# Optimization experiments

Hardware: AMD Instinct MI355X
Metric: run time of the kernel (lower is better)

The kernel has to match this reference:

```python
import jax, jax.numpy as jnp
import numpy as np

NUM_HEADS = 16

def setup_inputs() -> dict:
    key = jax.random.key(0)
    k1, k2, k3 = jax.random.split(key, 3)
    B, N, C = 4, 4096, 1024
    x = jax.random.normal(k1, (B, N, C), dtype=jnp.float32)
    y = jax.random.normal(k2, (B, N, C), dtype=jnp.float32)
    # nn.Linear(embed_dim, embed_dim): weight [C, C], bias [C]
    W_proj = jax.random.normal(k3, (C, C), dtype=jnp.float32) * (1.0 / np.sqrt(C))
    b_proj = jnp.zeros((C,), dtype=jnp.float32)
    return {"x": x, "y": y, "W_proj": W_proj, "b_proj": b_proj}

def reference(x, y, W_proj, b_proj):
    B, N, C = x.shape
    H = NUM_HEADS
    d = C // H
    # NOTE: no head transpose in the original -> scores are over the HEAD axis.
    q = x.reshape(B, N, H, d)
    k = y.reshape(B, N, H, d)
    v = y.reshape(B, N, H, d)
    # attn: [B, N, H, H], per-token head-to-head scores
    attn = jnp.einsum('bnhd,bngd->bnhg', q, k) / jnp.sqrt(jnp.asarray(d, x.dtype))
    attn = jax.nn.softmax(attn, axis=-1)
    # dropout(p=0.1) is identity in eval mode
    o = jnp.einsum('bnhg,bngd->bnhd', attn, v)          # [B, N, H, d]
    # x.transpose(1, 2).reshape(B, N, C) in torch:
    o = jnp.transpose(o, (0, 2, 1, 3)).reshape(B, N, C)
    out = o @ W_proj.T + b_proj
    return out
```

## Files before the change

### kernel.cpp

```cpp
#include <hip/hip_runtime.h>
#include <hip/hip_bf16.h>
#include <stdint.h>

typedef __attribute__((ext_vector_type(8))) short bf16x8;
typedef __attribute__((ext_vector_type(4))) short bf16x4;
typedef __attribute__((ext_vector_type(4))) float f32x4;
typedef __attribute__((ext_vector_type(4))) int   i32x4;

static __device__ __forceinline__ short f2bs(float f) {
  __hip_bfloat16 h = __float2bfloat16(f);
  return __builtin_bit_cast(short, h);
}

__device__ __forceinline__ void gload_lds16(const void* g, void* l) {
  auto* gp = reinterpret_cast<__attribute__((address_space(1))) uint32_t*>((uintptr_t)g);
  auto* lp = reinterpret_cast<__attribute__((address_space(3))) uint32_t*>((uintptr_t)l);
  __builtin_amdgcn_global_load_lds(gp, lp, 16, 0, 0);
}

__global__ __launch_bounds__(256) void attn_kernel(
    const float* __restrict__ x, const float* __restrict__ y,
    __hip_bfloat16* __restrict__ A)
{
  const int wid  = threadIdx.x >> 6;
  const int lane = threadIdx.x & 63;
  const int tok  = blockIdx.x * 4 + wid;
  const int b    = tok >> 12;
  const int n    = tok & 4095;

  const float* xr = x + (size_t)tok * 1024;
  const float* yr = y + (size_t)tok * 1024;

  const int c  = lane & 15;
  const int qq = lane >> 4;

  const int fbase = c * 64 + qq * 8;
  bf16x8 yf[2], xf[2];
  #pragma unroll
  for (int kk = 0; kk < 2; ++kk) {
    const float4 a0 = *(const float4*)(yr + fbase + kk * 32);
    const float4 a1 = *(const float4*)(yr + fbase + kk * 32 + 4);
    const float4 b0 = *(const float4*)(xr + fbase + kk * 32);
    const float4 b1 = *(const float4*)(xr + fbase + kk * 32 + 4);
    yf[kk] = bf16x8{f2bs(a0.x), f2bs(a0.y), f2bs(a0.z), f2bs(a0.w),
                    f2bs(a1.x), f2bs(a1.y), f2bs(a1.z), f2bs(a1.w)};
    xf[kk] = bf16x8{f2bs(b0.x), f2bs(b0.y), f2bs(b0.z), f2bs(b0.w),
                    f2bs(b1.x), f2bs(b1.y), f2bs(b1.z), f2bs(b1.w)};
  }

  f32x4 acc = {0.f, 0.f, 0.f, 0.f};
  acc = __builtin_amdgcn_mfma_f32_16x16x32_bf16(yf[0], xf[0], acc, 0, 0, 0);
  acc = __builtin_amdgcn_mfma_f32_16x16x32_bf16(yf[1], xf[1], acc, 0, 0, 0);

  float sc[4];
  #pragma unroll
  for (int r = 0; r < 4; ++r) sc[r] = acc[r] * 0.125f;
  float mx = fmaxf(fmaxf(sc[0], sc[1]), fmaxf(sc[2], sc[3]));
  mx = fmaxf(mx, __shfl_xor(mx, 16));
  mx = fmaxf(mx, __shfl_xor(mx, 32));
  float e[4];
  #pragma unroll
  for (int r = 0; r < 4; ++r) e[r] = __expf(sc[r] - mx);
  float sm = (e[0] + e[1]) + (e[2] + e[3]);
  sm += __shfl_xor(sm, 16);
  sm += __shfl_xor(sm, 32);
  const float inv = 1.0f / sm;
  float p[4];
  #pragma unroll
  for (int r = 0; r < 4; ++r) p[r] = e[r] * inv;

  f32x4 o[4];
  #pragma unroll
  for (int q = 0; q < 4; ++q) o[q] = f32x4{0.f, 0.f, 0.f, 0.f};

#if __has_builtin(__builtin_amdgcn_mfma_f32_16x16x16bf16_1k)
  const bf16x4 pa = {f2bs(p[0]), f2bs(p[1]), f2bs(p[2]), f2bs(p[3])};
  #pragma unroll
  for (int q = 0; q < 4; ++q) {
    bf16x4 bq;
    #pragma unroll
    for (int j = 0; j < 4; ++j)
      bq[j] = f2bs(yr[(qq * 4 + j) * 64 + q * 16 + c]);
    o[q] = __builtin_amdgcn_mfma_f32_16x16x16bf16_1k(pa, bq, o[q], 0, 0, 0);
  }
#else
  const int u0 = ((int)(unsigned short)f2bs(p[1]) << 16) | (unsigned short)f2bs(p[0]);
  const int u1 = ((int)(unsigned short)f2bs(p[3]) << 16) | (unsigned short)f2bs(p[2]);
  const int s0 = c + 32 * qq;
  int a0 = __shfl(u0, s0), a1 = __shfl(u1, s0);
  int a2 = __shfl(u0, s0 + 16), a3 = __shfl(u1, s0 + 16);
  const bool valid = (qq < 2);
  if (!valid) { a0 = 0; a1 = 0; a2 = 0; a3 = 0; }
  const bf16x8 a8 = __builtin_bit_cast(bf16x8, i32x4{a0, a1, a2, a3});
  #pragma unroll
  for (int q = 0; q < 4; ++q) {
    bf16x8 b8;
    #pragma unroll
    for (int j = 0; j < 8; ++j) {
      const int g = (qq * 8 + j) & 15;
      const float v = yr[g * 64 + q * 16 + c];
      b8[j] = valid ? f2bs(v) : (short)0;
    }
    o[q] = __builtin_amdgcn_mfma_f32_16x16x32_bf16(a8, b8, o[q], 0, 0, 0);
  }
#endif

  const size_t base = ((size_t)b * 4096 + (n >> 4)) * 1024 + ((n & 15) << 6) + c;
  #pragma unroll
  for (int q = 0; q < 4; ++q)
    #pragma unroll
    for (int r = 0; r < 4; ++r) {
      const int h = qq * 4 + r;
      A[base + (size_t)h * 262144 + q * 16] = __float2bfloat16(o[q][r]);
    }
}

__global__ __launch_bounds__(256) void wcvt_kernel(const float* __restrict__ w,
                                                   __hip_bfloat16* __restrict__ wb)
{
  const int i = (blockIdx.x * 256 + threadIdx.x) * 4;
  const float4 v = *(const float4*)(w + i);
  wb[i + 0] = __float2bfloat16(v.x);
  wb[i + 1] = __float2bfloat16(v.y);
  wb[i + 2] = __float2bfloat16(v.z);
  wb[i + 3] = __float2bfloat16(v.w);
}

#define NT 32

#define FENCE asm volatile("" ::: "memory")
#define BAR   __builtin_amdgcn_s_barrier()
#define LGKM0 asm volatile("s_waitcnt lgkmcnt(0)" ::: "memory")
#define VM4   asm volatile("s_waitcnt vmcnt(4)" ::: "memory")
#define VM0   asm volatile("s_waitcnt vmcnt(0)" ::: "memory")
#define SB0   __builtin_amdgcn_sched_barrier(0)
#define SP1   __builtin_amdgcn_s_setprio(1)
#define SP0   __builtin_amdgcn_s_setprio(0)

#define STAGE(toff, bo) do {                                        \
    gload_lds16(aSrc + (toff),          aDst + (bo));               \
    gload_lds16(aSrc + (toff) + 131072, aDst + (bo) + 4096);        \
    gload_lds16(bSrc + (toff),          bDst + (bo));               \
    gload_lds16(bSrc + (toff) + 131072, bDst + (bo) + 4096);        \
  } while (0)

__global__ __launch_bounds__(256, 3) void gemm128(
    const __hip_bfloat16* __restrict__ A,
    const __hip_bfloat16* __restrict__ Bw,
    const float* __restrict__ bias,
    float* __restrict__ C)
{
  constexpr int K = 1024, Nn = 1024;
  __shared__ char ldsA[3 * 8192];
  __shared__ char ldsB[3 * 8192];

  const int tid  = threadIdx.x;
  const int lane = tid & 63;
  const int wid  = tid >> 6;
  const int wr   = wid >> 1;
  const int wcN  = wid & 1;

  const int bid = blockIdx.x;
  const int nb  = (bid & 7) * 128 + (bid >> 3);
  const int mBase = (nb >> 3) * 128;
  const int nBase = (nb & 7) * 128;

  const int srow = tid >> 2;
  const int lcb  = (((tid & 3) ^ ((tid >> 3) & 3)) << 4);
  const char* aSrc = (const char*)A  + (size_t)(mBase + srow) * (K * 2) + lcb;
  const char* bSrc = (const char*)Bw + (size_t)(nBase + srow) * (K * 2) + lcb;
  char* aDst = ldsA + tid * 16;
  char* bDst = ldsB + tid * 16;

  const int fr = lane & 15;
  const int kq = lane >> 4;
  const int ofk  = ((kq ^ ((fr >> 1) & 3)) << 4);
  const int aOff = (wr  * 64 + fr) * 64 + ofk;
  const int bOff = (wcN * 64 + fr) * 64 + ofk;

  f32x4 acc[4][4];
  #pragma unroll
  for (int m = 0; m < 4; ++m)
    #pragma unroll
    for (int n = 0; n < 4; ++n) acc[m][n] = f32x4{0.f, 0.f, 0.f, 0.f};

  STAGE(0, 0);
  STAGE(64, 8192);
  VM4; FENCE; BAR; FENCE;

  auto tile = [&](int t, int b0off, int b2off, int stg, int gate) {
    if (stg) STAGE((t + 2) * 64, b2off);
    bf16x8 Af[4], Bf[4];
    const char* aB = ldsA + b0off + aOff;
    const char* bB = ldsB + b0off + bOff;
    #pragma unroll
    for (int n = 0; n < 4; ++n) Bf[n] = *(const bf16x8*)(bB + n * 1024);
    #pragma unroll
    for (int m = 0; m < 4; ++m) Af[m] = *(const bf16x8*)(aB + m * 1024);
    LGKM0; SB0;
    SP1;
    #pragma unroll
    for (int m = 0; m < 4; ++m)
      #pragma unroll
      for (int n = 0; n < 4; ++n)
        acc[m][n] = __builtin_amdgcn_mfma_f32_16x16x32_bf16(Af[m], Bf[n], acc[m][n], 0, 0, 0);
    SP0;
    if (gate == 4) { VM4; }
    else if (gate == 0) { VM0; }
    FENCE; BAR; FENCE;
  };

  for (int t = 0; t < 30; t += 3) {
    tile(t,     0,     16384, 1, 4);
    tile(t + 1, 8192,  0,     1, 4);
    tile(t + 2, 16384, 8192,  1, 4);
  }
  tile(30, 0,    0, 0, 0);
  tile(31, 8192, 0, 0, -1);

  const int fq = lane >> 4;
  #pragma unroll
  for (int n = 0; n < 4; ++n) {
    const int col = nBase + wcN * 64 + n * 16 + fr;
    const float bv = bias[col];
    #pragma unroll
    for (int m = 0; m < 4; ++m) {
      const int row0 = mBase + wr * 64 + m * 16 + fq * 4;
      #pragma unroll
      for (int r = 0; r < 4; ++r)
        C[(size_t)(row0 + r) * Nn + col] = acc[m][n][r] + bv;
    }
  }
}

extern "C" void kernel_launch(void* const* d_in, const int* in_sizes, int n_in,
                              void* d_out, int out_size, void* d_ws, size_t ws_size,
                              hipStream_t stream) {
  const float* x    = (const float*)d_in[0];
  const float* y    = (const float*)d_in[1];
  const float* W    = (const float*)d_in[2];
  const float* bias = (const float*)d_in[3];
  float* out = (float*)d_out;

  __hip_bfloat16* Abuf = (__hip_bfloat16*)d_ws;
  __hip_bfloat16* Wbuf = (__hip_bfloat16*)((char*)d_ws + (size_t)16384 * 1024 * 2);

  wcvt_kernel<<<1024, 256, 0, stream>>>(W, Wbuf);
  attn_kernel<<<4096, 256, 0, stream>>>(x, y, Abuf);
  gemm128<<<1024, 256, 0, stream>>>(Abuf, Wbuf, bias, out);
}
```

Before: 80.11 us.

## Fuse weight conversion into attention kernel and make GEMM blocks cover two M tiles

```diff
diff --git a/kernel.cpp b/kernel.cpp
--- a/kernel.cpp
+++ b/kernel.cpp
@@ -20,8 +20,18 @@
 
 __global__ __launch_bounds__(256) void attn_kernel(
     const float* __restrict__ x, const float* __restrict__ y,
-    __hip_bfloat16* __restrict__ A)
+    __hip_bfloat16* __restrict__ A,
+    const float* __restrict__ W, __hip_bfloat16* __restrict__ Wb)
 {
+  if (blockIdx.x < 1024) {
+    const int i = (blockIdx.x * 256 + threadIdx.x) * 4;
+    const float4 v = *(const float4*)(W + i);
+    Wb[i + 0] = __float2bfloat16(v.x);
+    Wb[i + 1] = __float2bfloat16(v.y);
+    Wb[i + 2] = __float2bfloat16(v.z);
+    Wb[i + 3] = __float2bfloat16(v.w);
+  }
+
   const int wid  = threadIdx.x >> 6;
   const int lane = threadIdx.x & 63;
   const int tok  = blockIdx.x * 4 + wid;
@@ -115,86 +125,92 @@
     }
 }
 
-__global__ __launch_bounds__(256) void wcvt_kernel(const float* __restrict__ w,
-                                                   __hip_bfloat16* __restrict__ wb)
-{
-  const int i = (blockIdx.x * 256 + threadIdx.x) * 4;
-  const float4 v = *(const float4*)(w + i);
-  wb[i + 0] = __float2bfloat16(v.x);
-  wb[i + 1] = __float2bfloat16(v.y);
-  wb[i + 2] = __float2bfloat16(v.z);
-  wb[i + 3] = __float2bfloat16(v.w);
-}
-
-#define NT 32
-
 #define FENCE asm volatile("" ::: "memory")
 #define BAR   __builtin_amdgcn_s_barrier()
 #define LGKM0 asm volatile("s_waitcnt lgkmcnt(0)" ::: "memory")
 #define VM4   asm volatile("s_waitcnt vmcnt(4)" ::: "memory")
+#define VM2   asm volatile("s_waitcnt vmcnt(2)" ::: "memory")
 #define VM0   asm volatile("s_waitcnt vmcnt(0)" ::: "memory")
 #define SB0   __builtin_amdgcn_sched_barrier(0)
 #define SP1   __builtin_amdgcn_s_setprio(1)
 #define SP0   __builtin_amdgcn_s_setprio(0)
 
-#define STAGE(toff, bo) do {                                        \
-    gload_lds16(aSrc + (toff),          aDst + (bo));               \
-    gload_lds16(aSrc + (toff) + 131072, aDst + (bo) + 4096);        \
-    gload_lds16(bSrc + (toff),          bDst + (bo));               \
-    gload_lds16(bSrc + (toff) + 131072, bDst + (bo) + 4096);        \
+#define STG(sp) do {                                                     \
+    const int kk_ = (sp) & 31;                                           \
+    const char* aS_ = ((sp) & 32) ? aS1 : aS0;                           \
+    gload_lds16(aS_ + kk_ * 64, aDst + (((sp) & 3) << 13));              \
+    gload_lds16(bS  + kk_ * 64, bDst + (((sp) & 3) << 13));              \
   } while (0)
 
-__global__ __launch_bounds__(256, 3) void gemm128(
+#define STORE_TILE(MB) do {                                              \
+    _Pragma("unroll")                                                    \
+    for (int n = 0; n < 2; ++n) {                                        \
+      const int col = nBase + wc * 32 + n * 16 + fr;                     \
+      const float bv = bias[col];                                        \
+      _Pragma("unroll")                                                  \
+      for (int m = 0; m < 4; ++m) {                                      \
+        const int row0 = (MB) + wr * 64 + m * 16 + fq * 4;               \
+        _Pragma("unroll")                                                \
+        for (int r = 0; r < 4; ++r)                                      \
+          C[(size_t)(row0 + r) * 1024 + col] = acc[m][n][r] + bv;        \
+      }                                                                  \
+    }                                                                    \
+  } while (0)
+
+__global__ __launch_bounds__(512, 4) void gemm_persist(
     const __hip_bfloat16* __restrict__ A,
     const __hip_bfloat16* __restrict__ Bw,
     const float* __restrict__ bias,
     float* __restrict__ C)
 {
-  constexpr int K = 1024, Nn = 1024;
-  __shared__ char ldsA[3 * 8192];
-  __shared__ char ldsB[3 * 8192];
+  __shared__ char ldsA[4 * 8192];
+  __shared__ char ldsB[4 * 8192];
 
   const int tid  = threadIdx.x;
   const int lane = tid & 63;
   const int wid  = tid >> 6;
-  const int wr   = wid >> 1;
-  const int wcN  = wid & 1;
-
-  const int bid = blockIdx.x;
-  const int nb  = (bid & 7) * 128 + (bid >> 3);
-  const int mBase = (nb >> 3) * 128;
-  const int nBase = (nb & 7) * 128;
+  const int wr   = wid >> 2;
+  const int wc   = wid & 3;
+
+  const int bid   = blockIdx.x;
+  const int nBase = (bid & 7) * 128;
+  const int mg    = bid >> 3;
+  const int mB0   = mg * 256;
+  const int mB1   = mB0 + 128;
 
   const int srow = tid >> 2;
-  const int lcb  = (((tid & 3) ^ ((tid >> 3) & 3)) << 4);
-  const char* aSrc = (const char*)A  + (size_t)(mBase + srow) * (K * 2) + lcb;
-  const char* bSrc = (const char*)Bw + (size_t)(nBase + srow) * (K * 2) + lcb;
+  const int lcb  = (((tid & 3) ^ ((srow >> 1) & 3)) << 4);
+  const char* aS0 = (const char*)A  + (size_t)(mB0 + srow) * 2048 + lcb;
+  const char* aS1 = (const char*)A  + (size_t)(mB1 + srow) * 2048 + lcb;
+  const char* bS  = (const char*)Bw + (size_t)(nBase + srow) * 2048 + lcb;
   char* aDst = ldsA + tid * 16;
   char* bDst = ldsB + tid * 16;
 
   const int fr = lane & 15;
   const int kq = lane >> 4;
+  const int fq = kq;
   const int ofk  = ((kq ^ ((fr >> 1) & 3)) << 4);
-  const int aOff = (wr  * 64 + fr) * 64 + ofk;
-  const int bOff = (wcN * 64 + fr) * 64 + ofk;
-
-  f32x4 acc[4][4];
+  const int aOff = (wr * 64 + fr) * 64 + ofk;
+  const int bOff = (wc * 32 + fr) * 64 + ofk;
+
+  f32x4 acc[4][2];
   #pragma unroll
   for (int m = 0; m < 4; ++m)
     #pragma unroll
-    for (int n = 0; n < 4; ++n) acc[m][n] = f32x4{0.f, 0.f, 0.f, 0.f};
-
-  STAGE(0, 0);
-  STAGE(64, 8192);
-  VM4; FENCE; BAR; FENCE;
-
-  auto tile = [&](int t, int b0off, int b2off, int stg, int gate) {
-    if (stg) STAGE((t + 2) * 64, b2off);
-    bf16x8 Af[4], Bf[4];
-    const char* aB = ldsA + b0off + aOff;
-    const char* bB = ldsB + b0off + bOff;
-    #pragma unroll
-    for (int n = 0; n < 4; ++n) Bf[n] = *(const bf16x8*)(bB + n * 1024);
+    for (int n = 0; n < 2; ++n) acc[m][n] = f32x4{0.f, 0.f, 0.f, 0.f};
+
+  STG(0); STG(1);
+
+  #pragma unroll 4
+  for (int s = 0; s < 64; ++s) {
+    if (s <= 61) { STG(s + 2); }
+    if (s <= 61) { VM4; } else if (s == 62) { VM2; } else { VM0; }
+    FENCE; BAR;
+    const char* aB = ldsA + ((s & 3) << 13) + aOff;
+    const char* bB = ldsB + ((s & 3) << 13) + bOff;
+    bf16x8 Af[4], Bf[2];
+    #pragma unroll
+    for (int n = 0; n < 2; ++n) Bf[n] = *(const bf16x8*)(bB + n * 1024);
     #pragma unroll
     for (int m = 0; m < 4; ++m) Af[m] = *(const bf16x8*)(aB + m * 1024);
     LGKM0; SB0;
@@ -202,35 +218,19 @@
     #pragma unroll
     for (int m = 0; m < 4; ++m)
       #pragma unroll
-      for (int n = 0; n < 4; ++n)
+      for (int n = 0; n < 2; ++n)
         acc[m][n] = __builtin_amdgcn_mfma_f32_16x16x32_bf16(Af[m], Bf[n], acc[m][n], 0, 0, 0);
     SP0;
-    if (gate == 4) { VM4; }
-    else if (gate == 0) { VM0; }
-    FENCE; BAR; FENCE;
-  };
-
-  for (int t = 0; t < 30; t += 3) {
-    tile(t,     0,     16384, 1, 4);
-    tile(t + 1, 8192,  0,     1, 4);
-    tile(t + 2, 16384, 8192,  1, 4);
-  }
-  tile(30, 0,    0, 0, 0);
-  tile(31, 8192, 0, 0, -1);
-
-  const int fq = lane >> 4;
-  #pragma unroll
-  for (int n = 0; n < 4; ++n) {
-    const int col = nBase + wcN * 64 + n * 16 + fr;
-    const float bv = bias[col];
-    #pragma unroll
-    for (int m = 0; m < 4; ++m) {
-      const int row0 = mBase + wr * 64 + m * 16 + fq * 4;
+    if (s == 31) {
+      STORE_TILE(mB0);
       #pragma unroll
-      for (int r = 0; r < 4; ++r)
-        C[(size_t)(row0 + r) * Nn + col] = acc[m][n][r] + bv;
+      for (int m = 0; m < 4; ++m)
+        #pragma unroll
+        for (int n = 0; n < 2; ++n) acc[m][n] = f32x4{0.f, 0.f, 0.f, 0.f};
     }
   }
+
+  STORE_TILE(mB1);
 }
 
 extern "C" void kernel_launch(void* const* d_in, const int* in_sizes, int n_in,
@@ -245,7 +245,6 @@
   __hip_bfloat16* Abuf = (__hip_bfloat16*)d_ws;
   __hip_bfloat16* Wbuf = (__hip_bfloat16*)((char*)d_ws + (size_t)16384 * 1024 * 2);
 
-  wcvt_kernel<<<1024, 256, 0, stream>>>(W, Wbuf);
-  attn_kernel<<<4096, 256, 0, stream>>>(x, y, Abuf);
-  gemm128<<<1024, 256, 0, stream>>>(Abuf, Wbuf, bias, out);
-}
+  attn_kernel<<<4096, 256, 0, stream>>>(x, y, Abuf, W, Wbuf);
+  gemm_persist<<<512, 512, 0, stream>>>(Abuf, Wbuf, bias, out);
+}
```

Result: slower. 88.45 us (+10.4%).

## Fuse weight conversion into attention kernel and enlarge GEMM tile to 256x128

Applied to the files above, without the earlier changes.

```diff
diff --git a/kernel.cpp b/kernel.cpp
--- a/kernel.cpp
+++ b/kernel.cpp
@@ -20,8 +20,18 @@
 
 __global__ __launch_bounds__(256) void attn_kernel(
     const float* __restrict__ x, const float* __restrict__ y,
-    __hip_bfloat16* __restrict__ A)
+    __hip_bfloat16* __restrict__ A,
+    const float* __restrict__ W, __hip_bfloat16* __restrict__ Wb)
 {
+  if (blockIdx.x < 1024) {
+    const int i = (blockIdx.x * 256 + threadIdx.x) * 4;
+    const float4 v = *(const float4*)(W + i);
+    Wb[i + 0] = __float2bfloat16(v.x);
+    Wb[i + 1] = __float2bfloat16(v.y);
+    Wb[i + 2] = __float2bfloat16(v.z);
+    Wb[i + 3] = __float2bfloat16(v.w);
+  }
+
   const int wid  = threadIdx.x >> 6;
   const int lane = threadIdx.x & 63;
   const int tok  = blockIdx.x * 4 + wid;
@@ -115,120 +125,111 @@
     }
 }
 
-__global__ __launch_bounds__(256) void wcvt_kernel(const float* __restrict__ w,
-                                                   __hip_bfloat16* __restrict__ wb)
-{
-  const int i = (blockIdx.x * 256 + threadIdx.x) * 4;
-  const float4 v = *(const float4*)(w + i);
-  wb[i + 0] = __float2bfloat16(v.x);
-  wb[i + 1] = __float2bfloat16(v.y);
-  wb[i + 2] = __float2bfloat16(v.z);
-  wb[i + 3] = __float2bfloat16(v.w);
-}
-
-#define NT 32
-
 #define FENCE asm volatile("" ::: "memory")
 #define BAR   __builtin_amdgcn_s_barrier()
 #define LGKM0 asm volatile("s_waitcnt lgkmcnt(0)" ::: "memory")
-#define VM4   asm volatile("s_waitcnt vmcnt(4)" ::: "memory")
+#define VM6   asm volatile("s_waitcnt vmcnt(6)" ::: "memory")
 #define VM0   asm volatile("s_waitcnt vmcnt(0)" ::: "memory")
 #define SB0   __builtin_amdgcn_sched_barrier(0)
 #define SP1   __builtin_amdgcn_s_setprio(1)
 #define SP0   __builtin_amdgcn_s_setprio(0)
 
-#define STAGE(toff, bo) do {                                        \
-    gload_lds16(aSrc + (toff),          aDst + (bo));               \
-    gload_lds16(aSrc + (toff) + 131072, aDst + (bo) + 4096);        \
-    gload_lds16(bSrc + (toff),          bDst + (bo));               \
-    gload_lds16(bSrc + (toff) + 131072, bDst + (bo) + 4096);        \
-  } while (0)
-
-__global__ __launch_bounds__(256, 3) void gemm128(
+__global__ __launch_bounds__(256, 2) void gemm_wt(
     const __hip_bfloat16* __restrict__ A,
     const __hip_bfloat16* __restrict__ Bw,
     const float* __restrict__ bias,
     float* __restrict__ C)
 {
-  constexpr int K = 1024, Nn = 1024;
-  __shared__ char ldsA[3 * 8192];
+  __shared__ char ldsA[3 * 16384];
   __shared__ char ldsB[3 * 8192];
 
   const int tid  = threadIdx.x;
   const int lane = tid & 63;
   const int wid  = tid >> 6;
   const int wr   = wid >> 1;
-  const int wcN  = wid & 1;
-
-  const int bid = blockIdx.x;
-  const int nb  = (bid & 7) * 128 + (bid >> 3);
-  const int mBase = (nb >> 3) * 128;
-  const int nBase = (nb & 7) * 128;
+  const int wc   = wid & 1;
+
+  const int bid   = blockIdx.x;
+  const int mg    = (bid & 7) | (((bid >> 3) & 7) << 3);
+  const int nt    = (bid >> 6) & 7;
+  const int mBase = mg * 256;
+  const int nBase = nt * 128;
 
   const int srow = tid >> 2;
-  const int lcb  = (((tid & 3) ^ ((tid >> 3) & 3)) << 4);
-  const char* aSrc = (const char*)A  + (size_t)(mBase + srow) * (K * 2) + lcb;
-  const char* bSrc = (const char*)Bw + (size_t)(nBase + srow) * (K * 2) + lcb;
-  char* aDst = ldsA + tid * 16;
-  char* bDst = ldsB + tid * 16;
+  const int lcb  = (((tid & 3) ^ ((srow >> 1) & 3)) << 4);
+  const char* aS0 = (const char*)A  + (size_t)(mBase + srow)       * 2048 + lcb;
+  const char* aS1 = (const char*)A  + (size_t)(mBase + 64 + srow)  * 2048 + lcb;
+  const char* aS2 = (const char*)A  + (size_t)(mBase + 128 + srow) * 2048 + lcb;
+  const char* aS3 = (const char*)A  + (size_t)(mBase + 192 + srow) * 2048 + lcb;
+  const char* bS0 = (const char*)Bw + (size_t)(nBase + srow)       * 2048 + lcb;
+  const char* bS1 = (const char*)Bw + (size_t)(nBase + 64 + srow)  * 2048 + lcb;
 
   const int fr = lane & 15;
   const int kq = lane >> 4;
+  const int fq = kq;
   const int ofk  = ((kq ^ ((fr >> 1) & 3)) << 4);
-  const int aOff = (wr  * 64 + fr) * 64 + ofk;
-  const int bOff = (wcN * 64 + fr) * 64 + ofk;
-
-  f32x4 acc[4][4];
-  #pragma unroll
-  for (int m = 0; m < 4; ++m)
+  const int aOff = (wr * 128 + fr) * 64 + ofk;
+  const int bOff = (wc * 64  + fr) * 64 + ofk;
+
+  f32x4 acc[8][4];
+  #pragma unroll
+  for (int m = 0; m < 8; ++m)
     #pragma unroll
     for (int n = 0; n < 4; ++n) acc[m][n] = f32x4{0.f, 0.f, 0.f, 0.f};
 
-  STAGE(0, 0);
-  STAGE(64, 8192);
-  VM4; FENCE; BAR; FENCE;
-
-  auto tile = [&](int t, int b0off, int b2off, int stg, int gate) {
-    if (stg) STAGE((t + 2) * 64, b2off);
-    bf16x8 Af[4], Bf[4];
-    const char* aB = ldsA + b0off + aOff;
-    const char* bB = ldsB + b0off + bOff;
+  auto STG = [&](int sp, int buf) {
+    const int ko = sp * 64;
+    char* aD = ldsA + buf * 16384 + tid * 16;
+    char* bD = ldsB + buf * 8192  + tid * 16;
+    gload_lds16(aS0 + ko, aD);
+    gload_lds16(aS1 + ko, aD + 4096);
+    gload_lds16(aS2 + ko, aD + 8192);
+    gload_lds16(aS3 + ko, aD + 12288);
+    gload_lds16(bS0 + ko, bD);
+    gload_lds16(bS1 + ko, bD + 4096);
+  };
+
+  auto STEP = [&](int s, int rb, bool stg, bool last) {
+    if (last) { VM0; } else { VM6; }
+    FENCE; BAR; FENCE;
+    if (stg) STG(s + 2, (s + 2) % 3);
+    const char* aB = ldsA + rb * 16384 + aOff;
+    const char* bB = ldsB + rb * 8192  + bOff;
+    bf16x8 Af[8], Bf[4];
     #pragma unroll
     for (int n = 0; n < 4; ++n) Bf[n] = *(const bf16x8*)(bB + n * 1024);
     #pragma unroll
-    for (int m = 0; m < 4; ++m) Af[m] = *(const bf16x8*)(aB + m * 1024);
+    for (int m = 0; m < 8; ++m) Af[m] = *(const bf16x8*)(aB + m * 1024);
     LGKM0; SB0;
     SP1;
     #pragma unroll
-    for (int m = 0; m < 4; ++m)
+    for (int m = 0; m < 8; ++m)
       #pragma unroll
       for (int n = 0; n < 4; ++n)
         acc[m][n] = __builtin_amdgcn_mfma_f32_16x16x32_bf16(Af[m], Bf[n], acc[m][n], 0, 0, 0);
     SP0;
-    if (gate == 4) { VM4; }
-    else if (gate == 0) { VM0; }
-    FENCE; BAR; FENCE;
   };
 
+  STG(0, 0); STG(1, 1);
+
   for (int t = 0; t < 30; t += 3) {
-    tile(t,     0,     16384, 1, 4);
-    tile(t + 1, 8192,  0,     1, 4);
-    tile(t + 2, 16384, 8192,  1, 4);
-  }
-  tile(30, 0,    0, 0, 0);
-  tile(31, 8192, 0, 0, -1);
-
-  const int fq = lane >> 4;
+    STEP(t,     0, true, false);
+    STEP(t + 1, 1, true, false);
+    STEP(t + 2, 2, true, false);
+  }
+  STEP(30, 0, false, false);
+  STEP(31, 1, false, true);
+
   #pragma unroll
   for (int n = 0; n < 4; ++n) {
-    const int col = nBase + wcN * 64 + n * 16 + fr;
+    const int col = nBase + wc * 64 + n * 16 + fr;
     const float bv = bias[col];
     #pragma unroll
-    for (int m = 0; m < 4; ++m) {
-      const int row0 = mBase + wr * 64 + m * 16 + fq * 4;
+    for (int m = 0; m < 8; ++m) {
+      const int row0 = mBase + wr * 128 + m * 16 + fq * 4;
       #pragma unroll
       for (int r = 0; r < 4; ++r)
-        C[(size_t)(row0 + r) * Nn + col] = acc[m][n][r] + bv;
+        C[(size_t)(row0 + r) * 1024 + col] = acc[m][n][r] + bv;
     }
   }
 }
@@ -245,7 +246,6 @@
   __hip_bfloat16* Abuf = (__hip_bfloat16*)d_ws;
   __hip_bfloat16* Wbuf = (__hip_bfloat16*)((char*)d_ws + (size_t)16384 * 1024 * 2);
 
-  wcvt_kernel<<<1024, 256, 0, stream>>>(W, Wbuf);
-  attn_kernel<<<4096, 256, 0, stream>>>(x, y, Abuf);
-  gemm128<<<1024, 256, 0, stream>>>(Abuf, Wbuf, bias, out);
-}
+  attn_kernel<<<4096, 256, 0, stream>>>(x, y, Abuf, W, Wbuf);
+  gemm_wt<<<512, 256, 0, stream>>>(Abuf, Wbuf, bias, out);
+}
```

Measured after the change: 73.84 us, median of 2. 7.8% less time.
